# Kernel tuning notes

Hardware: AMD Instinct MI355X
Metric: run time of the kernel (lower is better)

The kernel has to match this reference:

```python
import jax, jax.numpy as jnp
import numpy as np

DECAY = 0.6
THRESH = 0.6
MASK_T = 784 * 4  # default T in create_general_mask


def _make_mask(dim, c_min=10, c_max=50, min_dc=0.95, max_dc=0.99, T=MASK_T):
    # Faithful numpy port of create_general_mask (phase_shift_max=0.0 -> no shift).
    dcs = np.linspace(min_dc, max_dc, dim)
    cycles = np.linspace(c_min, c_max, dim)
    rows = []
    for cyc, dc in zip(cycles, dcs):
        cyc = int(np.ceil(cyc))
        on = int(np.ceil(dc * cyc))
        pat = [1] * on + [0] * (cyc - on)
        full = pat * (T // cyc) + pat[: T % cyc]
        rows.append(full)
    return jnp.asarray(np.array(rows, dtype=np.float32))  # [dim, T]


def setup_inputs() -> dict:
    key = jax.random.key(0)
    k1, k2, k3, k4, k5 = jax.random.split(key, 5)
    T, B, NTOKEN, NINP, H1, H2 = 128, 32, 32000, 256, 512, 512
    raw_input = jax.random.randint(k1, (T, B), 0, NTOKEN)
    enc_w = jax.random.uniform(k2, (NTOKEN, NINP), jnp.float32, -0.1, 0.1)
    # kaiming_uniform-like init: bound = sqrt(6 / fan_in), torch fan_in = dim 1
    b1 = float(np.sqrt(6.0 / H1))
    b2 = float(np.sqrt(6.0 / H2))
    fc1 = jax.random.uniform(k3, (NINP, H1), jnp.float32, -b1, b1)
    fc2 = jax.random.uniform(k4, (H1, H2), jnp.float32, -b2, b2)
    dec_w = jax.random.uniform(k5, (NTOKEN, H2), jnp.float32, -0.1, 0.1)
    dec_b = jnp.zeros((NTOKEN,), jnp.float32)
    mask1 = _make_mask(H1)
    mask2 = _make_mask(H2)
    return {"raw_input": raw_input, "enc_w": enc_w, "fc1": fc1, "fc2": fc2,
            "dec_w": dec_w, "dec_b": dec_b, "mask1": mask1, "mask2": mask2}


def _act(x):
    # ActFun.forward: heaviside spike
    return (x > 0.0).astype(x.dtype)


def reference(raw_input, enc_w, fc1, fc2, dec_w, dec_b, mask1, mask2):
    T, B = raw_input.shape
    emb = enc_w[raw_input]                    # [T, B, ninp] (dropout p=0 -> identity)
    m1 = mask1[:, :T].T                       # [T, H1]
    m2 = mask2[:, :T].T                       # [T, H2]

    def rhythm_update(fc, x, mem, m):
        state = x @ fc                        # [B, H]
        reset = (mem > THRESH).astype(x.dtype)
        new_mem = mem * (1.0 - reset) * DECAY + state
        mem = jnp.where(m == 0.0, mem, new_mem)   # mask broadcasts [H] -> [B, H]
        spike = _act(mem - THRESH) * m
        return mem, spike

    h1 = jnp.zeros((B, fc1.shape[1]), emb.dtype)
    h2 = jnp.zeros((B, fc2.shape[1]), emb.dtype)

    def step(carry, xs):
        h1m, h2m = carry
        x, ma, mb = xs
        h1m, s1 = rhythm_update(fc1, x, h1m, ma)
        h2m, s2 = rhythm_update(fc2, s1, h2m, mb)
        return (h1m, h2m), s2

    _, spikes = jax.lax.scan(step, (h1, h2), (emb, m1, m2))  # [T, B, H2]
    decoded = spikes @ dec_w.T + dec_b        # [T, B, ntoken]
    return decoded
```

## Files before the change

### kernel.cpp

```cpp
#include <hip/hip_runtime.h>


typedef __attribute__((ext_vector_type(8))) short short8;
typedef __attribute__((ext_vector_type(4))) float f32x4;
typedef __attribute__((ext_vector_type(8))) unsigned short us8;

#define WAITVM(N) asm volatile("s_waitcnt vmcnt(" #N ")" ::: "memory")

__device__ __forceinline__ unsigned short f2bf(float f) {
    unsigned int u = __float_as_uint(f);
    unsigned int r = (u + 0x7FFFu + ((u >> 16) & 1u)) >> 16;
    return (unsigned short)r;
}

__global__ __launch_bounds__(256) void maskT_kernel(
    const float* __restrict__ m1, const float* __restrict__ m2,
    float* __restrict__ t1, float* __restrict__ t2)
{
    int i = blockIdx.x * 256 + threadIdx.x;
    int h = i >> 7, t = i & 127;
    t1[t * 512 + h] = m1[(size_t)h * 3136 + t];
    t2[t * 512 + h] = m2[(size_t)h * 3136 + t];
}

__global__ __launch_bounds__(256) void split_kernel(
    const float* __restrict__ w, unsigned short* __restrict__ w2, int n4)
{
    int i = blockIdx.x * 256 + threadIdx.x;
    if (i >= n4) return;
    float4 v = ((const float4*)w)[i];
    float vv[4] = {v.x, v.y, v.z, v.w};
    us8 o;
    #pragma unroll
    for (int c = 0; c < 4; ++c) {
        unsigned short hb = f2bf(vv[c]);
        float hf = __uint_as_float(((unsigned int)hb) << 16);
        o[2 * c]     = hb;
        o[2 * c + 1] = f2bf(vv[c] - hf);
    }
    ((us8*)w2)[i] = o;
}

__global__ __launch_bounds__(256) void gemm_f32_kernel(
    const float* __restrict__ A, const float* __restrict__ B,
    float* __restrict__ C, int M, int N, int K,
    const int* __restrict__ gidx, const float* __restrict__ gtable)
{
    __shared__ float As[16][64];
    __shared__ float Bs[16][64];
    int tid = threadIdx.x;
    int bn0 = blockIdx.x * 64, bm0 = blockIdx.y * 64;

    int lrowA = tid >> 2;
    int lkA   = (tid & 3) * 4;
    int lkB   = tid >> 4;
    int lnB   = (tid & 15) * 4;
    int ty = tid >> 4, tx = tid & 15;

    const float* Abase;
    size_t aoff;
    int grow = bm0 + lrowA;
    if (gidx) { Abase = gtable; aoff = (size_t)gidx[grow] * K; }
    else      { Abase = A;      aoff = (size_t)grow * K; }

    float acc[4][4];
    #pragma unroll
    for (int i = 0; i < 4; ++i)
        #pragma unroll
        for (int j = 0; j < 4; ++j) acc[i][j] = 0.f;

    for (int k0 = 0; k0 < K; k0 += 16) {
        float4 av = *(const float4*)(Abase + aoff + k0 + lkA);
        As[lkA + 0][lrowA] = av.x;
        As[lkA + 1][lrowA] = av.y;
        As[lkA + 2][lrowA] = av.z;
        As[lkA + 3][lrowA] = av.w;
        float4 bv = *(const float4*)(B + (size_t)(k0 + lkB) * N + bn0 + lnB);
        *(float4*)&Bs[lkB][lnB] = bv;
        __syncthreads();
        #pragma unroll
        for (int kk = 0; kk < 16; ++kk) {
            float4 aq = *(float4*)&As[kk][ty * 4];
            float4 bq = *(float4*)&Bs[kk][tx * 4];
            float aa[4] = {aq.x, aq.y, aq.z, aq.w};
            float bb[4] = {bq.x, bq.y, bq.z, bq.w};
            #pragma unroll
            for (int i = 0; i < 4; ++i)
                #pragma unroll
                for (int j = 0; j < 4; ++j) acc[i][j] += aa[i] * bb[j];
        }
        __syncthreads();
    }
    #pragma unroll
    for (int i = 0; i < 4; ++i) {
        float4 v = {acc[i][0], acc[i][1], acc[i][2], acc[i][3]};
        *(float4*)(C + (size_t)(bm0 + ty * 4 + i) * N + bn0 + tx * 4) = v;
    }
}

template <int DUP>
__global__ __launch_bounds__(64) void scan_kernel(
    const float* __restrict__ state, const float* __restrict__ maskT,
    float* __restrict__ outF, unsigned int* __restrict__ outU)
{
    int tid = blockIdx.x * 64 + threadIdx.x;
    int b = tid >> 9, h = tid & 511;
    float mem = 0.f;
    #pragma unroll 8
    for (int t = 0; t < 128; ++t) {
        size_t ridx = (size_t)(t * 32 + b) * 512 + h;
        float st = state[ridx];
        float m  = maskT[t * 512 + h];
        float nm = (mem > 0.6f) ? st : mem * 0.6f + st;
        mem = (m == 0.0f) ? mem : nm;
        float spf = (mem > 0.6f) ? m : 0.0f;
        if (DUP) outU[ridx] = f2bf(spf) * 0x10001u;
        else     outF[ridx] = spf;
    }
}

__global__ __launch_bounds__(512, 2) void gemm3_kernel(
    const unsigned short* __restrict__ A,
    const unsigned short* __restrict__ W,
    const float* __restrict__ bias, float* __restrict__ C)
{
    constexpr int K = 1024, NTOK = 32000;
    __shared__ char lds[131072];

    int tid  = threadIdx.x;
    int lane = tid & 63;
    int wid  = __builtin_amdgcn_readfirstlane(tid >> 6);

    int bid = blockIdx.x;
    int swz = (bid & 7) * 250 + (bid >> 3);
    int mt = swz & 15;
    int nt = swz >> 4;
    int m0 = mt * 256, n0 = nt * 256;

    int wm = wid >> 2, wn = wid & 3;

    const unsigned short* srcB[4];
    int dstOff[4];
    #pragma unroll
    for (int i = 0; i < 4; ++i) {
        int q   = i * 512 + tid;
        int isB = q >> 10;
        int qq  = q & 1023;
        int row = qq >> 2;
        int cp  = qq & 3;
        int c   = cp ^ ((row + (row >> 2)) & 3);
        srcB[i] = (isB ? W + (size_t)(n0 + row) * K
                       : A + (size_t)(m0 + row) * K) + c * 8;
        dstOff[i] = (i * 512 + wid * 64) * 16;
    }

    int r = lane & 15, co = lane >> 4;
    int aOff[8], bOff[4];
    #pragma unroll
    for (int mf = 0; mf < 8; ++mf) {
        int row = wm * 128 + mf * 16 + r;
        aOff[mf] = row * 64 + ((co ^ ((row + (row >> 2)) & 3)) * 16);
    }
    #pragma unroll
    for (int nf = 0; nf < 4; ++nf) {
        int row = wn * 64 + nf * 16 + r;
        bOff[nf] = 16384 + row * 64 + ((co ^ ((row + (row >> 2)) & 3)) * 16);
    }

    f32x4 acc[8][4];
    #pragma unroll
    for (int i = 0; i < 8; ++i)
        #pragma unroll
        for (int j = 0; j < 4; ++j) acc[i][j] = (f32x4){0.f, 0.f, 0.f, 0.f};

    auto STAGE = [&](int slot, int kt) {
        #pragma unroll
        for (int i = 0; i < 4; ++i) {
            __builtin_amdgcn_global_load_lds(
                (const __attribute__((address_space(1))) unsigned int*)(srcB[i] + kt * 32),
                (__attribute__((address_space(3))) unsigned int*)(lds + (slot << 15) + dstOff[i]),
                16, 0, 0);
        }
    };
    auto COMPUTE = [&](int t) {
        const char* base = lds + ((t & 3) << 15);
        short8 fa[8], fb[4];
        #pragma unroll
        for (int mf = 0; mf < 8; ++mf) fa[mf] = *(const short8*)(base + aOff[mf]);
        #pragma unroll
        for (int nf = 0; nf < 4; ++nf) fb[nf] = *(const short8*)(base + bOff[nf]);
        __builtin_amdgcn_s_setprio(1);
        #pragma unroll
        for (int mf = 0; mf < 8; ++mf)
            #pragma unroll
            for (int nf = 0; nf < 4; ++nf)
                acc[mf][nf] = __builtin_amdgcn_mfma_f32_16x16x32_bf16(
                    fa[mf], fb[nf], acc[mf][nf], 0, 0, 0);
        __builtin_amdgcn_s_setprio(0);
    };

    STAGE(0, 0);
    STAGE(1, 1);
    STAGE(2, 2);
    WAITVM(8);
    __builtin_amdgcn_s_barrier();
    __builtin_amdgcn_sched_barrier(0);

    #pragma unroll 4
    for (int t = 0; t < 29; ++t) {
        STAGE((t + 3) & 3, t + 3);
        COMPUTE(t);
        WAITVM(8);
        __builtin_amdgcn_s_barrier();
        __builtin_amdgcn_sched_barrier(0);
    }
    COMPUTE(29);
    WAITVM(4);
    __builtin_amdgcn_s_barrier();
    __builtin_amdgcn_sched_barrier(0);
    COMPUTE(30);
    WAITVM(0);
    __builtin_amdgcn_s_barrier();
    __builtin_amdgcn_sched_barrier(0);
    COMPUTE(31);

    int lr = lane >> 4, lc = lane & 15;
    #pragma unroll
    for (int nf = 0; nf < 4; ++nf) {
        int gc = n0 + wn * 64 + nf * 16 + lc;
        float bv = bias[gc];
        #pragma unroll
        for (int mf = 0; mf < 8; ++mf) {
            int gr = m0 + wm * 128 + mf * 16 + lr * 4;
            f32x4 v = acc[mf][nf];
            #pragma unroll
            for (int j = 0; j < 4; ++j)
                C[(size_t)(gr + j) * NTOK + gc] = v[j] + bv;
        }
    }
}

extern "C" void kernel_launch(void* const* d_in, const int* in_sizes, int n_in,
                              void* d_out, int out_size, void* d_ws, size_t ws_size,
                              hipStream_t stream)
{
    const int*   raw   = (const int*)  d_in[0];
    const float* enc_w = (const float*)d_in[1];
    const float* fc1   = (const float*)d_in[2];
    const float* fc2   = (const float*)d_in[3];
    const float* dec_w = (const float*)d_in[4];
    const float* dec_b = (const float*)d_in[5];
    const float* mask1 = (const float*)d_in[6];
    const float* mask2 = (const float*)d_in[7];
    float* out = (float*)d_out;

    const int H1 = 512, H2 = 512, NINP = 256, NTOK = 32000;
    const int M = 128 * 32;

    char* ws = (char*)d_ws;
    float*          st  = (float*)ws;
    float*          spF = (float*)(ws + (size_t)(8u << 20));
    unsigned int*   a2u = (unsigned int*)(ws + (size_t)(8u << 20));
    unsigned short* A2  = (unsigned short*)(ws + (size_t)(8u << 20));
    unsigned short* W2  = (unsigned short*)(ws + (size_t)(16u << 20));
    float* mT1 = (float*)d_out;
    float* mT2 = (float*)d_out + 65536;

    maskT_kernel<<<256, 256, 0, stream>>>(mask1, mask2, mT1, mT2);

    int n4 = NTOK * H2 / 4;
    split_kernel<<<(n4 + 255) / 256, 256, 0, stream>>>(dec_w, W2, n4);

    gemm_f32_kernel<<<dim3(H1 / 64, M / 64), 256, 0, stream>>>(
        nullptr, fc1, st, M, H1, NINP, raw, enc_w);

    scan_kernel<0><<<256, 64, 0, stream>>>(st, mT1, spF, nullptr);

    gemm_f32_kernel<<<dim3(H2 / 64, M / 64), 256, 0, stream>>>(
        spF, fc2, st, M, H2, H1, nullptr, nullptr);

    scan_kernel<1><<<256, 64, 0, stream>>>(st, mT2, nullptr, a2u);

    gemm3_kernel<<<(M / 256) * (NTOK / 256), 512, 0, stream>>>(A2, W2, dec_b, out);

    (void)in_sizes; (void)n_in; (void)out_size; (void)ws_size;
}
```

Baseline: 964.2 us.

## Split GEMM K-step into two phases with interleaved loads and new LDS swizzle

```diff
diff --git a/kernel.cpp b/kernel.cpp
--- a/kernel.cpp
+++ b/kernel.cpp
@@ -6,6 +6,7 @@
 typedef __attribute__((ext_vector_type(8))) unsigned short us8;
 
 #define WAITVM(N) asm volatile("s_waitcnt vmcnt(" #N ")" ::: "memory")
+#define LGKM0()   asm volatile("s_waitcnt lgkmcnt(0)" ::: "memory")
 
 __device__ __forceinline__ unsigned short f2bf(float f) {
     unsigned int u = __float_as_uint(f);
@@ -106,16 +107,22 @@
     int tid = blockIdx.x * 64 + threadIdx.x;
     int b = tid >> 9, h = tid & 511;
     float mem = 0.f;
-    #pragma unroll 8
-    for (int t = 0; t < 128; ++t) {
-        size_t ridx = (size_t)(t * 32 + b) * 512 + h;
-        float st = state[ridx];
-        float m  = maskT[t * 512 + h];
-        float nm = (mem > 0.6f) ? st : mem * 0.6f + st;
-        mem = (m == 0.0f) ? mem : nm;
-        float spf = (mem > 0.6f) ? m : 0.0f;
-        if (DUP) outU[ridx] = f2bf(spf) * 0x10001u;
-        else     outF[ridx] = spf;
+    for (int t0 = 0; t0 < 128; t0 += 8) {
+        float st8[8], m8[8];
+        #pragma unroll
+        for (int u = 0; u < 8; ++u) {
+            st8[u] = state[(size_t)((t0 + u) * 32 + b) * 512 + h];
+            m8[u]  = maskT[(t0 + u) * 512 + h];
+        }
+        #pragma unroll
+        for (int u = 0; u < 8; ++u) {
+            float nm = (mem > 0.6f) ? st8[u] : mem * 0.6f + st8[u];
+            mem = (m8[u] == 0.0f) ? mem : nm;
+            float spf = (mem > 0.6f) ? m8[u] : 0.0f;
+            size_t ridx = (size_t)((t0 + u) * 32 + b) * 512 + h;
+            if (DUP) outU[ridx] = f2bf(spf) * 0x10001u;
+            else     outF[ridx] = spf;
+        }
     }
 }
 
@@ -146,11 +153,12 @@
         int q   = i * 512 + tid;
         int isB = q >> 10;
         int qq  = q & 1023;
-        int row = qq >> 2;
-        int cp  = qq & 3;
-        int c   = cp ^ ((row + (row >> 2)) & 3);
+        int j   = qq >> 3;
+        int cp  = qq & 7;
+        int c   = cp ^ (j & 7);
+        int row = 2 * j + (c >> 2);
         srcB[i] = (isB ? W + (size_t)(n0 + row) * K
-                       : A + (size_t)(m0 + row) * K) + c * 8;
+                       : A + (size_t)(m0 + row) * K) + (c & 3) * 8;
         dstOff[i] = (i * 512 + wid * 64) * 16;
     }
 
@@ -159,12 +167,14 @@
     #pragma unroll
     for (int mf = 0; mf < 8; ++mf) {
         int row = wm * 128 + mf * 16 + r;
-        aOff[mf] = row * 64 + ((co ^ ((row + (row >> 2)) & 3)) * 16);
+        int j = row >> 1, c = co + 4 * (row & 1);
+        aOff[mf] = (j * 8 + (c ^ (j & 7))) * 16;
     }
     #pragma unroll
     for (int nf = 0; nf < 4; ++nf) {
         int row = wn * 64 + nf * 16 + r;
-        bOff[nf] = 16384 + row * 64 + ((co ^ ((row + (row >> 2)) & 3)) * 16);
+        int j = row >> 1, c = co + 4 * (row & 1);
+        bOff[nf] = 16384 + (j * 8 + (c ^ (j & 7))) * 16;
     }
 
     f32x4 acc[8][4];
@@ -173,56 +183,66 @@
         #pragma unroll
         for (int j = 0; j < 4; ++j) acc[i][j] = (f32x4){0.f, 0.f, 0.f, 0.f};
 
-    auto STAGE = [&](int slot, int kt) {
-        #pragma unroll
-        for (int i = 0; i < 4; ++i) {
-            __builtin_amdgcn_global_load_lds(
-                (const __attribute__((address_space(1))) unsigned int*)(srcB[i] + kt * 32),
-                (__attribute__((address_space(3))) unsigned int*)(lds + (slot << 15) + dstOff[i]),
-                16, 0, 0);
-        }
+    auto GLOAD = [&](int i, int kt) {
+        __builtin_amdgcn_global_load_lds(
+            (const __attribute__((address_space(1))) unsigned int*)(srcB[i] + kt * 32),
+            (__attribute__((address_space(3))) unsigned int*)(lds + ((kt & 3) << 15) + dstOff[i]),
+            16, 0, 0);
     };
-    auto COMPUTE = [&](int t) {
+
+    auto STEP = [&](int t, bool stage) {
         const char* base = lds + ((t & 3) << 15);
-        short8 fa[8], fb[4];
-        #pragma unroll
-        for (int mf = 0; mf < 8; ++mf) fa[mf] = *(const short8*)(base + aOff[mf]);
-        #pragma unroll
-        for (int nf = 0; nf < 4; ++nf) fb[nf] = *(const short8*)(base + bOff[nf]);
+        short8 fa0[4], fb[4], fa1[4];
+        if (stage) { GLOAD(0, t + 3); GLOAD(1, t + 3); }
+        #pragma unroll
+        for (int f = 0; f < 4; ++f) fa0[f] = *(const short8*)(base + aOff[f]);
+        #pragma unroll
+        for (int f = 0; f < 4; ++f) fb[f]  = *(const short8*)(base + bOff[f]);
+        __builtin_amdgcn_s_barrier();
+        LGKM0();
         __builtin_amdgcn_s_setprio(1);
         #pragma unroll
-        for (int mf = 0; mf < 8; ++mf)
+        for (int mf = 0; mf < 4; ++mf)
             #pragma unroll
             for (int nf = 0; nf < 4; ++nf)
                 acc[mf][nf] = __builtin_amdgcn_mfma_f32_16x16x32_bf16(
-                    fa[mf], fb[nf], acc[mf][nf], 0, 0, 0);
+                    fa0[mf], fb[nf], acc[mf][nf], 0, 0, 0);
+        __builtin_amdgcn_s_setprio(0);
+        __builtin_amdgcn_s_barrier();
+        if (stage) { GLOAD(2, t + 3); GLOAD(3, t + 3); }
+        #pragma unroll
+        for (int f = 0; f < 4; ++f) fa1[f] = *(const short8*)(base + aOff[4 + f]);
+        __builtin_amdgcn_s_barrier();
+        LGKM0();
+        __builtin_amdgcn_s_setprio(1);
+        #pragma unroll
+        for (int mf = 0; mf < 4; ++mf)
+            #pragma unroll
+            for (int nf = 0; nf < 4; ++nf)
+                acc[4 + mf][nf] = __builtin_amdgcn_mfma_f32_16x16x32_bf16(
+                    fa1[mf], fb[nf], acc[4 + mf][nf], 0, 0, 0);
         __builtin_amdgcn_s_setprio(0);
     };
 
-    STAGE(0, 0);
-    STAGE(1, 1);
-    STAGE(2, 2);
+    #pragma unroll
+    for (int kt = 0; kt < 3; ++kt)
+        #pragma unroll
+        for (int i = 0; i < 4; ++i) GLOAD(i, kt);
     WAITVM(8);
     __builtin_amdgcn_s_barrier();
-    __builtin_amdgcn_sched_barrier(0);
-
-    #pragma unroll 4
+
     for (int t = 0; t < 29; ++t) {
-        STAGE((t + 3) & 3, t + 3);
-        COMPUTE(t);
+        STEP(t, true);
         WAITVM(8);
         __builtin_amdgcn_s_barrier();
-        __builtin_amdgcn_sched_barrier(0);
-    }
-    COMPUTE(29);
+    }
+    STEP(29, false);
     WAITVM(4);
     __builtin_amdgcn_s_barrier();
-    __builtin_amdgcn_sched_barrier(0);
-    COMPUTE(30);
+    STEP(30, false);
     WAITVM(0);
     __builtin_amdgcn_s_barrier();
-    __builtin_amdgcn_sched_barrier(0);
-    COMPUTE(31);
+    STEP(31, false);
 
     int lr = lane >> 4, lc = lane & 15;
     #pragma unroll
```

New measurement: 932.5 us. -3.3%, faster.
